# Optimization experiments

Measured on AMD Instinct MI355X. Metric: run time of the kernel, lower is better.

The kernel has to match this reference:

```python
import jax, jax.numpy as jnp
import numpy as np

C = 512        # concept_num
D = 256        # input_dim / embedding_dim
H = 512        # msg_hidden_dim
M = 256        # msg_output_dim
OH = 512       # hidden_dim
T = 2          # edge_type_num
E = C * (C - 1)  # fully-connected graph without self-loops = 261632


def _glorot(key, shape, fan_in):
    return jax.random.normal(key, shape, jnp.float32) / np.sqrt(fan_in).astype(np.float32)


def setup_inputs() -> dict:
    key = jax.random.key(0)
    ks = jax.random.split(key, 12)
    inputs = jax.random.normal(ks[0], (C, D), jnp.float32)
    rel_type = jax.random.uniform(ks[1], (E, T), jnp.float32)
    send_idx = jax.random.randint(ks[2], (E,), 0, C, jnp.int32)
    rec_idx = jax.random.randint(ks[3], (E,), 0, C, jnp.int32)
    # per-edge-type message MLP params, stacked over type dim
    W1 = _glorot(ks[4], (T, 2 * D, H), 2 * D)
    b1 = jnp.zeros((T, H), jnp.float32)
    W2 = _glorot(ks[5], (T, H, M), H)
    b2 = jnp.zeros((T, M), jnp.float32)
    # output MLP params
    Wo1 = _glorot(ks[6], (M, OH), M)
    bo1 = jnp.zeros((OH,), jnp.float32)
    Wo2 = _glorot(ks[7], (OH, OH), OH)
    bo2 = jnp.zeros((OH,), jnp.float32)
    Wo3 = _glorot(ks[8], (OH, D), OH)
    bo3 = jnp.zeros((D,), jnp.float32)
    return {"inputs": inputs, "rel_type": rel_type, "W1": W1, "b1": b1,
            "W2": W2, "b2": b2, "Wo1": Wo1, "bo1": bo1, "Wo2": Wo2,
            "bo2": bo2, "Wo3": Wo3, "bo3": bo3,
            "send_idx": send_idx, "rec_idx": rec_idx}


def reference(inputs, rel_type, W1, b1, W2, b2, Wo1, bo1, Wo2, bo2, Wo3, bo3,
              send_idx, rec_idx):
    # node2edge: one-hot sparse matmul == index gather
    senders = jnp.take(inputs, send_idx, axis=0)      # [E, D]
    receivers = jnp.take(inputs, rec_idx, axis=0)     # [E, D]
    pre_msg = jnp.concatenate([senders, receivers], axis=-1)  # [E, 2D]
    # per-edge-type MLPs, weighted-summed by rel_type (dropout=0 / eval mode)
    all_msgs = jnp.zeros((pre_msg.shape[0], M), jnp.float32)
    for i in range(T):
        msg = jax.nn.relu(pre_msg @ W1[i] + b1[i])    # [E, H]
        msg = jax.nn.relu(msg @ W2[i] + b2[i])        # [E, M]
        all_msgs = all_msgs + msg * rel_type[:, i:i + 1]
    # edge2node: transposed one-hot sparse matmul == scatter-add over receivers
    agg_msgs = jax.ops.segment_sum(all_msgs, rec_idx, num_segments=inputs.shape[0])  # [C, M]
    pred = jax.nn.relu(agg_msgs @ Wo1 + bo1)
    pred = jax.nn.relu(pred @ Wo2 + bo2)
    return pred @ Wo3 + bo3                           # [C, D]
```

## Files before the change

kernel.cpp:

```cpp
#include <hip/hip_runtime.h>

#define C_N   512
#define E_N   261632

typedef _Float16 f16;
typedef _Float16 f16x8_t __attribute__((ext_vector_type(8)));
typedef float    f32x16_t __attribute__((ext_vector_type(16)));

__global__ __launch_bounds__(256) void k_prep(const float* __restrict__ inputs,
    const float* __restrict__ W1, const float* __restrict__ b1,
    const float* __restrict__ W2, const int* __restrict__ rec,
    const float* __restrict__ Wo1, const float* __restrict__ Wo2, const float* __restrict__ Wo3,
    f16* __restrict__ SA, f16* __restrict__ RB, f16* __restrict__ W2p,
    f16* __restrict__ Wo1p, f16* __restrict__ Wo2p, f16* __restrict__ Wo3p,
    int* __restrict__ hist_part)
{
  int bid = blockIdx.x;
  if (bid < 256) {
    int t  = bid >> 7;
    int c0 = (bid & 127) * 4;
    __shared__ float xs[4][256];
    for (int i = threadIdx.x; i < 1024; i += 256)
      xs[i >> 8][i & 255] = inputs[(size_t)(c0 + (i >> 8)) * 256 + (i & 255)];
    __syncthreads();
    const float* W1t = W1 + (size_t)t * 512 * 512;
    int h0 = threadIdx.x;
    float sa[2][4] = {{0.f}}, rbv[2][4] = {{0.f}};
    #pragma unroll 4
    for (int d = 0; d < 256; d++) {
      float wt0 = W1t[d * 512 + h0];
      float wt1 = W1t[d * 512 + h0 + 256];
      float wb0 = W1t[(256 + d) * 512 + h0];
      float wb1 = W1t[(256 + d) * 512 + h0 + 256];
      #pragma unroll
      for (int r = 0; r < 4; r++) {
        float x = xs[r][d];
        sa[0][r]  += x * wt0; sa[1][r]  += x * wt1;
        rbv[0][r] += x * wb0; rbv[1][r] += x * wb1;
      }
    }
    #pragma unroll
    for (int hh = 0; hh < 2; hh++) {
      int h = h0 + hh * 256;
      float bb = b1[t * 512 + h];
      #pragma unroll
      for (int r = 0; r < 4; r++) {
        SA[((size_t)(t * 512 + c0 + r)) * 512 + h] = (f16)sa[hh][r];
        RB[((size_t)(t * 512 + c0 + r)) * 512 + h] = (f16)(rbv[hh][r] + bb);
      }
    }
  } else if (bid < 384) {
    int gid  = (bid - 256) * 256 + threadIdx.x;
    int lane = gid & 63;
    int ct   = (gid >> 6) & 7;
    int kc   = (gid >> 9) & 31;
    int t    = gid >> 14;
    int n    = ct * 32 + (lane & 31);
    int k0   = kc * 16 + (lane >> 5) * 8;
    const float* src = W2 + (size_t)t * 512 * 256;
    f16x8_t v;
    #pragma unroll
    for (int j = 0; j < 8; j++) v[j] = (f16)src[(size_t)(k0 + j) * 256 + n];
    *(f16x8_t*)(W2p + (size_t)gid * 8) = v;
  } else if (bid < 448) {
    int hb = bid - 384;
    __shared__ int lh[512];
    for (int i = threadIdx.x; i < 512; i += 256) lh[i] = 0;
    __syncthreads();
    int e0 = hb * (E_N / 64);
    for (int i = threadIdx.x; i < E_N / 64; i += 256)
      atomicAdd(&lh[rec[e0 + i]], 1);
    __syncthreads();
    for (int i = threadIdx.x; i < 512; i += 256)
      hist_part[hb * 512 + i] = lh[i];
  } else if (bid < 512) {
    int gid  = (bid - 448) * 256 + threadIdx.x;
    int lane = gid & 63;
    int ct   = (gid >> 6) & 15;
    int kc   = gid >> 10;
    int n    = ct * 32 + (lane & 31);
    int k0   = kc * 16 + (lane >> 5) * 8;
    f16x8_t v;
    #pragma unroll
    for (int j = 0; j < 8; j++) v[j] = (f16)Wo1[(size_t)(k0 + j) * 512 + n];
    *(f16x8_t*)(Wo1p + (size_t)gid * 8) = v;
  } else if (bid < 640) {
    int gid  = (bid - 512) * 256 + threadIdx.x;
    int lane = gid & 63;
    int ct   = (gid >> 6) & 15;
    int kc   = gid >> 10;
    int n    = ct * 32 + (lane & 31);
    int k0   = kc * 16 + (lane >> 5) * 8;
    f16x8_t v;
    #pragma unroll
    for (int j = 0; j < 8; j++) v[j] = (f16)Wo2[(size_t)(k0 + j) * 512 + n];
    *(f16x8_t*)(Wo2p + (size_t)gid * 8) = v;
  } else {
    int gid  = (bid - 640) * 256 + threadIdx.x;
    int lane = gid & 63;
    int ct   = (gid >> 6) & 7;
    int kc   = gid >> 9;
    int n    = ct * 32 + (lane & 31);
    int k0   = kc * 16 + (lane >> 5) * 8;
    f16x8_t v;
    #pragma unroll
    for (int j = 0; j < 8; j++) v[j] = (f16)Wo3[(size_t)(k0 + j) * 256 + n];
    *(f16x8_t*)(Wo3p + (size_t)gid * 8) = v;
  }
}

__global__ void k_scan(const int* __restrict__ hist_part, int* __restrict__ seg,
                       int* __restrict__ base)
{
  __shared__ int s[512];
  int tid = threadIdx.x;
  int tot = 0;
  #pragma unroll 8
  for (int b = 0; b < 64; b++) tot += hist_part[b * 512 + tid];
  s[tid] = tot;
  __syncthreads();
  for (int off = 1; off < 512; off <<= 1) {
    int v = (tid >= off) ? s[tid - off] : 0;
    __syncthreads();
    s[tid] += v;
    __syncthreads();
  }
  int excl = s[tid] - tot;
  seg[tid] = excl;
  if (tid == 0) seg[512] = E_N;
  int run = excl;
  for (int b = 0; b < 64; b++) {
    base[b * 512 + tid] = run;
    run += hist_part[b * 512 + tid];
  }
}

__global__ __launch_bounds__(1024) void k_scatter3(const int* __restrict__ rec,
    const int* __restrict__ send, const float* __restrict__ rel,
    const int* __restrict__ base, int* __restrict__ ssend, float2* __restrict__ srel)
{
  __shared__ int lh[512];
  __shared__ int lb[512];
  int b = blockIdx.x;
  int e0 = b * (E_N / 64);
  for (int i = threadIdx.x; i < 512; i += 1024) { lh[i] = 0; lb[i] = base[b * 512 + i]; }
  __syncthreads();
  for (int i = threadIdx.x; i < E_N / 64; i += 1024) {
    int e = e0 + i;
    int r = rec[e];
    int p = lb[r] + atomicAdd(&lh[r], 1);
    ssend[p] = send[e];
    srel[p]  = make_float2(rel[2 * (size_t)e], rel[2 * (size_t)e + 1]);
  }
}

#define H1S 520

__global__ __launch_bounds__(512, 2) void k_edges(
    const f16* __restrict__ SA, const f16* __restrict__ RB,
    const f16* __restrict__ W2p, const float* __restrict__ b2,
    const int* __restrict__ ssend, const float2* __restrict__ srel,
    const int* __restrict__ seg, float* __restrict__ agg)
{
  __shared__ f16   h1[128 * H1S];
  __shared__ f16   rbs[2][512];
  __shared__ float b2s[2][256];
  __shared__ float aggL[256];
  __shared__ float relv2[2][128][2];
  __shared__ int   sends2[2][128];

  int c    = blockIdx.x;
  int tid  = threadIdx.x;
  int lane = tid & 63;
  int w    = tid >> 6;
  int hlf  = lane >> 5;
  int l31  = lane & 31;
  int q    = tid & 63;
  int rb0  = tid >> 6;

  if (tid < 128) {
    int t = tid >> 6, qq = tid & 63;
    *(f16x8_t*)&rbs[t][qq * 8] = *(const f16x8_t*)&RB[((size_t)(t * 512 + c)) * 512 + qq * 8];
  }
  if (tid < 256) aggL[tid] = 0.0f;
  { int t = (tid >> 8) & 1, col = tid & 255; b2s[t][col] = b2[t * 256 + col]; }

  int s0 = seg[c], s1 = seg[c + 1];
  int nt = (s1 - s0 + 127) >> 7;

  if (nt > 0 && tid < 128) {
    int pos = s0 + tid;
    if (pos < s1) {
      sends2[0][tid] = ssend[pos];
      float2 rr = srel[pos];
      relv2[0][tid][0] = rr.x;
      relv2[0][tid][1] = rr.y;
    } else {
      sends2[0][tid] = 0; relv2[0][tid][0] = 0.f; relv2[0][tid][1] = 0.f;
    }
  }
  __syncthreads();

  f16x8_t g[16];
  const f16x8_t* SAc = (const f16x8_t*)SA;
  const f16x8_t* Bp  = (const f16x8_t*)W2p;

  if (nt > 0) {
    #pragma unroll
    for (int j = 0; j < 16; j++)
      g[j] = SAc[(size_t)sends2[0][rb0 + 8 * j] * 64 + q];
  }

  for (int ph = 0; ph < 2 * nt; ph++) {
    int ti  = ph >> 1;
    int t   = ph & 1;
    int cb  = ti & 1;
    int nb  = cb ^ 1;
    bool more = (ti + 1 < nt);

    {
      f16x8_t rbq = *(const f16x8_t*)&rbs[t][q * 8];
      #pragma unroll
      for (int j = 0; j < 16; j++) {
        int row = rb0 + 8 * j;
        f16x8_t hv;
        #pragma unroll
        for (int e = 0; e < 8; e++) {
          f16 v = (f16)(g[j][e] + rbq[e]);
          hv[e] = (v > (f16)0.0f) ? v : (f16)0.0f;
        }
        *(f16x8_t*)&h1[row * H1S + q * 8] = hv;
      }
    }
    __syncthreads();

    if (t == 0 && more && tid < 128) {
      int pos = s0 + (ti + 1) * 128 + tid;
      if (pos < s1) {
        sends2[nb][tid] = ssend[pos];
        float2 rr = srel[pos];
        relv2[nb][tid][0] = rr.x;
        relv2[nb][tid][1] = rr.y;
      } else {
        sends2[nb][tid] = 0; relv2[nb][tid][0] = 0.f; relv2[nb][tid][1] = 0.f;
      }
    }

    f32x16_t acc[4];
    #pragma unroll
    for (int rt = 0; rt < 4; rt++)
      #pragma unroll
      for (int r = 0; r < 16; r++) acc[rt][r] = 0.f;

    f16x8_t bb[2];
    bb[0] = Bp[(size_t)(((t * 32 + 0) * 8 + w) * 64 + lane)];
    bb[1] = Bp[(size_t)(((t * 32 + 1) * 8 + w) * 64 + lane)];

    if (t == 0) {
      #pragma unroll
      for (int j = 0; j < 16; j++)
        g[j] = SAc[(size_t)(512 + sends2[cb][rb0 + 8 * j]) * 64 + q];
    } else if (more) {
      #pragma unroll
      for (int j = 0; j < 16; j++)
        g[j] = SAc[(size_t)sends2[nb][rb0 + 8 * j] * 64 + q];
    }

    for (int kc = 0; kc < 32; kc++) {
      int pb = kc & 1;
      #pragma unroll
      for (int rt = 0; rt < 4; rt++) {
        f16x8_t af = *(const f16x8_t*)&h1[(rt * 32 + l31) * H1S + kc * 16 + hlf * 8];
        acc[rt] = __builtin_amdgcn_mfma_f32_32x32x16_f16(af, bb[pb], acc[rt], 0, 0, 0);
      }
      if (kc + 2 < 32)
        bb[pb] = Bp[(size_t)(((t * 32 + kc + 2) * 8 + w) * 64 + lane)];
    }

    {
      int col = w * 32 + l31;
      float b2c = b2s[t][col];
      float csum = 0.0f;
      #pragma unroll
      for (int rt = 0; rt < 4; rt++)
        #pragma unroll
        for (int r = 0; r < 16; r++) {
          int row = rt * 32 + (r & 3) + 8 * (r >> 2) + 4 * hlf;
          float v = fmaxf(acc[rt][r] + b2c, 0.0f);
          csum += v * relv2[cb][row][t];
        }
      csum += __shfl_xor(csum, 32, 64);
      if (hlf == 0) aggL[col] += csum;
    }
    __syncthreads();
  }

  if (tid < 256) agg[(size_t)c * 256 + tid] = aggL[tid];
}

__global__ __launch_bounds__(256) void k_omlp1(const float* __restrict__ agg,
    const f16* __restrict__ Wo1p, const float* __restrict__ bo1, f16* __restrict__ h1o)
{
  int tid = threadIdx.x, lane = tid & 63, w = tid >> 6;
  int hlf = lane >> 5, l31 = lane & 31;
  int br = blockIdx.x, bc = blockIdx.y;
  f32x16_t acc[2][2];
  #pragma unroll
  for (int rt = 0; rt < 2; rt++)
    #pragma unroll
    for (int ctl = 0; ctl < 2; ctl++)
      #pragma unroll
      for (int r = 0; r < 16; r++) acc[rt][ctl][r] = 0.f;
  for (int kc = 0; kc < 16; kc++) {
    f16x8_t af[2];
    #pragma unroll
    for (int rt = 0; rt < 2; rt++) {
      const float4* p = (const float4*)&agg[(size_t)(br * 64 + rt * 32 + l31) * 256 + kc * 16 + hlf * 8];
      float4 u0 = p[0], u1 = p[1];
      af[rt] = (f16x8_t){(f16)u0.x, (f16)u0.y, (f16)u0.z, (f16)u0.w,
                         (f16)u1.x, (f16)u1.y, (f16)u1.z, (f16)u1.w};
    }
    #pragma unroll
    for (int ctl = 0; ctl < 2; ctl++) {
      f16x8_t bfr = *(const f16x8_t*)&Wo1p[((size_t)(kc * 16 + bc * 8 + 2 * w + ctl) * 64 + lane) * 8];
      #pragma unroll
      for (int rt = 0; rt < 2; rt++)
        acc[rt][ctl] = __builtin_amdgcn_mfma_f32_32x32x16_f16(af[rt], bfr, acc[rt][ctl], 0, 0, 0);
    }
  }
  #pragma unroll
  for (int ctl = 0; ctl < 2; ctl++) {
    int col = bc * 256 + (2 * w + ctl) * 32 + l31;
    float bias = bo1[col];
    #pragma unroll
    for (int rt = 0; rt < 2; rt++)
      #pragma unroll
      for (int r = 0; r < 16; r++) {
        int row = br * 64 + rt * 32 + (r & 3) + 8 * (r >> 2) + 4 * hlf;
        h1o[(size_t)row * 512 + col] = (f16)fmaxf(acc[rt][ctl][r] + bias, 0.f);
      }
  }
}

__global__ __launch_bounds__(256) void k_omlp2(const f16* __restrict__ h1o,
    const f16* __restrict__ Wo2p, const float* __restrict__ bo2, f16* __restrict__ h2o)
{
  int tid = threadIdx.x, lane = tid & 63, w = tid >> 6;
  int hlf = lane >> 5, l31 = lane & 31;
  int br = blockIdx.x, bc = blockIdx.y;
  f32x16_t acc[2][2];
  #pragma unroll
  for (int rt = 0; rt < 2; rt++)
    #pragma unroll
    for (int ctl = 0; ctl < 2; ctl++)
      #pragma unroll
      for (int r = 0; r < 16; r++) acc[rt][ctl][r] = 0.f;
  for (int kc = 0; kc < 32; kc++) {
    f16x8_t af[2];
    #pragma unroll
    for (int rt = 0; rt < 2; rt++)
      af[rt] = *(const f16x8_t*)&h1o[(size_t)(br * 64 + rt * 32 + l31) * 512 + kc * 16 + hlf * 8];
    #pragma unroll
    for (int ctl = 0; ctl < 2; ctl++) {
      f16x8_t bfr = *(const f16x8_t*)&Wo2p[((size_t)(kc * 16 + bc * 8 + 2 * w + ctl) * 64 + lane) * 8];
      #pragma unroll
      for (int rt = 0; rt < 2; rt++)
        acc[rt][ctl] = __builtin_amdgcn_mfma_f32_32x32x16_f16(af[rt], bfr, acc[rt][ctl], 0, 0, 0);
    }
  }
  #pragma unroll
  for (int ctl = 0; ctl < 2; ctl++) {
    int col = bc * 256 + (2 * w + ctl) * 32 + l31;
    float bias = bo2[col];
    #pragma unroll
    for (int rt = 0; rt < 2; rt++)
      #pragma unroll
      for (int r = 0; r < 16; r++) {
        int row = br * 64 + rt * 32 + (r & 3) + 8 * (r >> 2) + 4 * hlf;
        h2o[(size_t)row * 512 + col] = (f16)fmaxf(acc[rt][ctl][r] + bias, 0.f);
      }
  }
}

__global__ __launch_bounds__(256) void k_omlp3(const f16* __restrict__ h2o,
    const f16* __restrict__ Wo3p, const float* __restrict__ bo3, float* __restrict__ out)
{
  int tid = threadIdx.x, lane = tid & 63, w = tid >> 6;
  int hlf = lane >> 5, l31 = lane & 31;
  int br = blockIdx.x;
  f32x16_t acc[2][2];
  #pragma unroll
  for (int rt = 0; rt < 2; rt++)
    #pragma unroll
    for (int ctl = 0; ctl < 2; ctl++)
      #pragma unroll
      for (int r = 0; r < 16; r++) acc[rt][ctl][r] = 0.f;
  for (int kc = 0; kc < 32; kc++) {
    f16x8_t af[2];
    #pragma unroll
    for (int rt = 0; rt < 2; rt++)
      af[rt] = *(const f16x8_t*)&h2o[(size_t)(br * 64 + rt * 32 + l31) * 512 + kc * 16 + hlf * 8];
    #pragma unroll
    for (int ctl = 0; ctl < 2; ctl++) {
      f16x8_t bfr = *(const f16x8_t*)&Wo3p[((size_t)(kc * 8 + 2 * w + ctl) * 64 + lane) * 8];
      #pragma unroll
      for (int rt = 0; rt < 2; rt++)
        acc[rt][ctl] = __builtin_amdgcn_mfma_f32_32x32x16_f16(af[rt], bfr, acc[rt][ctl], 0, 0, 0);
    }
  }
  #pragma unroll
  for (int ctl = 0; ctl < 2; ctl++) {
    int col = (2 * w + ctl) * 32 + l31;
    float bias = bo3[col];
    #pragma unroll
    for (int rt = 0; rt < 2; rt++)
      #pragma unroll
      for (int r = 0; r < 16; r++) {
        int row = br * 64 + rt * 32 + (r & 3) + 8 * (r >> 2) + 4 * hlf;
        out[(size_t)row * 256 + col] = acc[rt][ctl][r] + bias;
      }
  }
}

extern "C" void kernel_launch(void* const* d_in, const int* in_sizes, int n_in,
                              void* d_out, int out_size, void* d_ws, size_t ws_size,
                              hipStream_t stream)
{
  (void)in_sizes; (void)n_in; (void)out_size; (void)ws_size;
  const float* inputs = (const float*)d_in[0];
  const float* rel    = (const float*)d_in[1];
  const float* W1     = (const float*)d_in[2];
  const float* b1     = (const float*)d_in[3];
  const float* W2     = (const float*)d_in[4];
  const float* b2     = (const float*)d_in[5];
  const float* Wo1    = (const float*)d_in[6];
  const float* bo1    = (const float*)d_in[7];
  const float* Wo2    = (const float*)d_in[8];
  const float* bo2    = (const float*)d_in[9];
  const float* Wo3    = (const float*)d_in[10];
  const float* bo3    = (const float*)d_in[11];
  const int* send_idx = (const int*)d_in[12];
  const int* rec_idx  = (const int*)d_in[13];
  float* out = (float*)d_out;

  char* ws = (char*)d_ws;
  f16*    SA        = (f16*)   (ws);
  f16*    RB        = (f16*)   (ws + (1u << 20));
  f16*    W2p       = (f16*)   (ws + (2u << 20));
  float*  agg       = (float*) (ws + (2560u << 10));
  int*    hist_part = (int*)   (ws + (3u << 20));
  int*    seg       = (int*)   (ws + (3u << 20) + (128u << 10));
  int*    base      = (int*)   (ws + (3u << 20) + (132u << 10));
  int*    ssend     = (int*)   (ws + (3584u << 10));
  float2* srel      = (float2*)(ws + (4608u << 10));
  f16*    Wo1p      = (f16*)   (ws + (6656u << 10));
  f16*    Wo2p      = (f16*)   (ws + (6912u << 10));
  f16*    Wo3p      = (f16*)   (ws + (7424u << 10));
  f16*    h1o       = (f16*)   (ws + (7680u << 10));
  f16*    h2o       = (f16*)   (ws + (8192u << 10));

  k_prep    <<<dim3(704), dim3(256),  0, stream>>>(inputs, W1, b1, W2, rec_idx,
                                                   Wo1, Wo2, Wo3,
                                                   SA, RB, W2p, Wo1p, Wo2p, Wo3p, hist_part);
  k_scan    <<<dim3(1),   dim3(512),  0, stream>>>(hist_part, seg, base);
  k_scatter3<<<dim3(64),  dim3(1024), 0, stream>>>(rec_idx, send_idx, rel, base, ssend, srel);
  k_edges   <<<dim3(512), dim3(512),  0, stream>>>(SA, RB, W2p, b2, ssend, srel, seg, agg);
  k_omlp1   <<<dim3(8,2), dim3(256),  0, stream>>>(agg, Wo1p, bo1, h1o);
  k_omlp2   <<<dim3(8,2), dim3(256),  0, stream>>>(h1o, Wo2p, bo2, h2o);
  k_omlp3   <<<dim3(8),   dim3(256),  0, stream>>>(h2o, Wo3p, bo3, out);
}
```

Before: 346.6 us.

## Split H1 K-dimension into halves to shrink LDS tile and raise occupancy

The per-block h1 shared-memory tile is halved by processing the 512-wide hidden dimension in two 256-wide K halves, with accumulators carried across the halves. Each thread now gathers 8 instead of 16 fp16 vectors, which cuts register use and LDS footprint, and launch bounds move from 2 to 4 blocks per CU. The cost is twice as many phases and barriers per tile, plus extra SA gathers for the second half.

```diff
diff --git a/kernel.cpp b/kernel.cpp
--- a/kernel.cpp
+++ b/kernel.cpp
@@ -154,15 +154,15 @@
   }
 }
 
-#define H1S 520
-
-__global__ __launch_bounds__(512, 2) void k_edges(
+#define H1S2 264
+
+__global__ __launch_bounds__(512, 4) void k_edges(
     const f16* __restrict__ SA, const f16* __restrict__ RB,
     const f16* __restrict__ W2p, const float* __restrict__ b2,
     const int* __restrict__ ssend, const float2* __restrict__ srel,
     const int* __restrict__ seg, float* __restrict__ agg)
 {
-  __shared__ f16   h1[128 * H1S];
+  __shared__ f16   h1[128 * H1S2];
   __shared__ f16   rbs[2][512];
   __shared__ float b2s[2][256];
   __shared__ float aggL[256];
@@ -175,8 +175,8 @@
   int w    = tid >> 6;
   int hlf  = lane >> 5;
   int l31  = lane & 31;
-  int q    = tid & 63;
-  int rb0  = tid >> 6;
+  int q5   = tid & 31;
+  int rb0  = tid >> 5;
 
   if (tid < 128) {
     int t = tid >> 6, qq = tid & 63;
@@ -201,40 +201,42 @@
   }
   __syncthreads();
 
-  f16x8_t g[16];
+  f16x8_t g[8];
   const f16x8_t* SAc = (const f16x8_t*)SA;
   const f16x8_t* Bp  = (const f16x8_t*)W2p;
+  f32x16_t acc[4];
 
   if (nt > 0) {
     #pragma unroll
-    for (int j = 0; j < 16; j++)
-      g[j] = SAc[(size_t)sends2[0][rb0 + 8 * j] * 64 + q];
-  }
-
-  for (int ph = 0; ph < 2 * nt; ph++) {
-    int ti  = ph >> 1;
-    int t   = ph & 1;
+    for (int j = 0; j < 8; j++)
+      g[j] = SAc[(size_t)sends2[0][rb0 + 16 * j] * 64 + q5];
+  }
+
+  for (int ph = 0; ph < 4 * nt; ph++) {
+    int ti  = ph >> 2;
+    int t   = (ph >> 1) & 1;
+    int kh  = ph & 1;
     int cb  = ti & 1;
     int nb  = cb ^ 1;
     bool more = (ti + 1 < nt);
 
     {
-      f16x8_t rbq = *(const f16x8_t*)&rbs[t][q * 8];
-      #pragma unroll
-      for (int j = 0; j < 16; j++) {
-        int row = rb0 + 8 * j;
+      f16x8_t rbq = *(const f16x8_t*)&rbs[t][(kh * 32 + q5) * 8];
+      #pragma unroll
+      for (int j = 0; j < 8; j++) {
+        int row = rb0 + 16 * j;
         f16x8_t hv;
         #pragma unroll
         for (int e = 0; e < 8; e++) {
           f16 v = (f16)(g[j][e] + rbq[e]);
           hv[e] = (v > (f16)0.0f) ? v : (f16)0.0f;
         }
-        *(f16x8_t*)&h1[row * H1S + q * 8] = hv;
-      }
-    }
-    __syncthreads();
-
-    if (t == 0 && more && tid < 128) {
+        *(f16x8_t*)&h1[row * H1S2 + q5 * 8] = hv;
+      }
+    }
+    __syncthreads();
+
+    if (t == 0 && kh == 0 && more && tid < 128) {
       int pos = s0 + (ti + 1) * 128 + tid;
       if (pos < s1) {
         sends2[nb][tid] = ssend[pos];
@@ -246,38 +248,43 @@
       }
     }
 
-    f32x16_t acc[4];
-    #pragma unroll
-    for (int rt = 0; rt < 4; rt++)
-      #pragma unroll
-      for (int r = 0; r < 16; r++) acc[rt][r] = 0.f;
+    if (kh == 0) {
+      #pragma unroll
+      for (int rt = 0; rt < 4; rt++)
+        #pragma unroll
+        for (int r = 0; r < 16; r++) acc[rt][r] = 0.f;
+    }
 
     f16x8_t bb[2];
-    bb[0] = Bp[(size_t)(((t * 32 + 0) * 8 + w) * 64 + lane)];
-    bb[1] = Bp[(size_t)(((t * 32 + 1) * 8 + w) * 64 + lane)];
-
-    if (t == 0) {
-      #pragma unroll
-      for (int j = 0; j < 16; j++)
-        g[j] = SAc[(size_t)(512 + sends2[cb][rb0 + 8 * j]) * 64 + q];
+    bb[0] = Bp[(size_t)(((t * 32 + kh * 16 + 0) * 8 + w) * 64 + lane)];
+    bb[1] = Bp[(size_t)(((t * 32 + kh * 16 + 1) * 8 + w) * 64 + lane)];
+
+    if (kh == 0) {
+      #pragma unroll
+      for (int j = 0; j < 8; j++)
+        g[j] = SAc[(size_t)(t * 512 + sends2[cb][rb0 + 16 * j]) * 64 + 32 + q5];
+    } else if (t == 0) {
+      #pragma unroll
+      for (int j = 0; j < 8; j++)
+        g[j] = SAc[(size_t)(512 + sends2[cb][rb0 + 16 * j]) * 64 + q5];
     } else if (more) {
       #pragma unroll
-      for (int j = 0; j < 16; j++)
-        g[j] = SAc[(size_t)sends2[nb][rb0 + 8 * j] * 64 + q];
-    }
-
-    for (int kc = 0; kc < 32; kc++) {
+      for (int j = 0; j < 8; j++)
+        g[j] = SAc[(size_t)sends2[nb][rb0 + 16 * j] * 64 + q5];
+    }
+
+    for (int kc = 0; kc < 16; kc++) {
       int pb = kc & 1;
       #pragma unroll
       for (int rt = 0; rt < 4; rt++) {
-        f16x8_t af = *(const f16x8_t*)&h1[(rt * 32 + l31) * H1S + kc * 16 + hlf * 8];
+        f16x8_t af = *(const f16x8_t*)&h1[(rt * 32 + l31) * H1S2 + kc * 16 + hlf * 8];
         acc[rt] = __builtin_amdgcn_mfma_f32_32x32x16_f16(af, bb[pb], acc[rt], 0, 0, 0);
       }
-      if (kc + 2 < 32)
-        bb[pb] = Bp[(size_t)(((t * 32 + kc + 2) * 8 + w) * 64 + lane)];
-    }
-
-    {
+      if (kc + 2 < 16)
+        bb[pb] = Bp[(size_t)(((t * 32 + kh * 16 + kc + 2) * 8 + w) * 64 + lane)];
+    }
+
+    if (kh == 1) {
       int col = w * 32 + l31;
       float b2c = b2s[t][col];
       float csum = 0.0f;
```

New measurement: 332.1 us. 4.2% less time.
